# Performance work log

Measured on AMD Instinct MI355X. Metric: run time of the kernel, lower is better.

## Reference

```python
import jax, jax.numpy as jnp
import numpy as np

N_STATE = 1024
N_HEAD = 16
LENGTHS = np.array([512, 576, 640, 704, 768, 832, 896, 1024], dtype=np.int32)
BATCH = len(LENGTHS)
MAX_SEQLEN = int(LENGTHS.max())
N_CTX = int(LENGTHS.sum())


def setup_inputs() -> dict:
    key = jax.random.key(0)
    ks = jax.random.split(key, 8)
    d = N_STATE
    cu = np.concatenate([[0], np.cumsum(LENGTHS)]).astype(np.int32)
    return {
        "x": jax.random.normal(ks[0], (N_CTX, d), dtype=jnp.float32),
        "Wq": jax.random.normal(ks[1], (d, d), dtype=jnp.float32) * 0.02,
        "bq": jnp.zeros((d,), dtype=jnp.float32),
        "Wk": jax.random.normal(ks[2], (d, d), dtype=jnp.float32) * 0.02,
        "Wv": jax.random.normal(ks[3], (d, d), dtype=jnp.float32) * 0.02,
        "bv": jnp.zeros((d,), dtype=jnp.float32),
        "Wo": jax.random.normal(ks[4], (d, d), dtype=jnp.float32) * 0.02,
        "bo": jnp.zeros((d,), dtype=jnp.float32),
        "cu_seqlens": jnp.asarray(cu),
    }


def reference(x, Wq, bq, Wk, Wv, bv, Wo, bo, cu_seqlens):
    n_ctx, d = x.shape
    H, hd = N_HEAD, d // N_HEAD
    scale = hd ** -0.5
    B, S = BATCH, MAX_SEQLEN  # static pad shape

    # QKV projections (torch Linear convention: y = x @ W.T + b; key has no bias)
    q = (x @ Wq.T + bq).reshape(n_ctx, H, hd)
    k = (x @ Wk.T).reshape(n_ctx, H, hd)
    v = (x @ Wv.T + bv).reshape(n_ctx, H, hd)

    seqlens = cu_seqlens[1:] - cu_seqlens[:-1]          # [B]
    tok = jnp.arange(n_ctx)
    seg = jnp.searchsorted(cu_seqlens[1:], tok, side="right")  # [n_ctx] batch id
    pos = tok - cu_seqlens[seg]                          # [n_ctx] position in seq

    # scatter packed tokens into zero-padded [B, S, H, hd]
    qp = jnp.zeros((B, S, H, hd), q.dtype).at[seg, pos].set(q)
    kp = jnp.zeros((B, S, H, hd), k.dtype).at[seg, pos].set(k)
    vp = jnp.zeros((B, S, H, hd), v.dtype).at[seg, pos].set(v)

    valid = jnp.arange(S)[None, :] < seqlens[:, None]    # [B, S] key mask

    scores = jnp.einsum("bihd,bjhd->bhij", qp, kp) * scale   # [B, H, S, S]
    neg = -jnp.finfo(scores.dtype).max
    scores = jnp.where(valid[:, None, None, :], scores, neg)
    weights = jax.nn.softmax(scores, axis=-1)
    ctx = jnp.einsum("bhij,bjhd->bihd", weights, vp)         # [B, S, H, hd]

    # gather back to packed [n_ctx, d]
    packed = ctx[seg, pos].reshape(n_ctx, d)
    return packed @ Wo.T + bo
```

## Files before the change

### kernel.cpp

```cpp
#include <hip/hip_runtime.h>
#include <hip/hip_fp16.h>
#include <stdint.h>

#define NCTX 5952
#define NHEAD 16
#define NABLK 372
#define NWBLK 256

typedef _Float16 f16x8 __attribute__((ext_vector_type(8)));
typedef _Float16 f16x4 __attribute__((ext_vector_type(4)));
typedef float    f32x4 __attribute__((ext_vector_type(4)));

typedef const __attribute__((address_space(1))) void* gp1;
typedef __attribute__((address_space(3))) void* lp3;

__device__ __forceinline__ f32x4 mfma16(f16x8 a, f16x8 b, f32x4 c) {
    return __builtin_amdgcn_mfma_f32_16x16x32_f16(a, b, c, 0, 0, 0);
}

#define SBAR() do { __builtin_amdgcn_sched_barrier(0); \
                    __builtin_amdgcn_s_barrier();      \
                    __builtin_amdgcn_sched_barrier(0); } while (0)

__device__ const int kQT[9]    = {0, 4, 9, 14, 20, 26, 33, 40, 48};
__device__ const int kBASE8[8] = {0, 512, 1088, 1728, 2432, 3200, 4032, 4928};
__device__ const int kLEN[8]   = {512, 576, 640, 704, 768, 832, 896, 1024};


__global__ __launch_bounds__(256) void presplit_all(
    const float* __restrict__ x,
    const float* __restrict__ Wq, const float* __restrict__ Wk,
    const float* __restrict__ Wv, const float* __restrict__ Wo,
    _Float16* __restrict__ Ah, _Float16* __restrict__ Wh)
{
    constexpr int NAG = NABLK * 32 * 64;
    const int idx = blockIdx.x * 256 + threadIdx.x;
    const float* src;
    _Float16* dst;
    if (idx < NAG) {
        int chunk = idx >> 6, within = idx & 63;
        int t = chunk & 31, b = chunk >> 5;
        int rb = within >> 2, go = within & 3;
        int r = b * 16 + rb;
        int g = go ^ ((r >> 1) & 3);
        src = x + (size_t)r * 1024 + t * 32 + g * 8;
        dst = Ah + (size_t)idx * 8;
    } else {
        int i2 = idx - NAG;
        int chunk = i2 >> 6, within = i2 & 63;
        int t = chunk & 31, b = chunk >> 5;
        int rb = within >> 2, go = within & 3;
        int n = b * 16 + rb;
        int g = go ^ ((n >> 1) & 3);
        const float* s = (n < 1024) ? Wq : (n < 2048) ? Wk : (n < 3072) ? Wv : Wo;
        src = s + (size_t)(n & 1023) * 1024 + t * 32 + g * 8;
        dst = Wh + (size_t)i2 * 8;
    }
    f32x4 v0 = *(const f32x4*)src;
    f32x4 v1 = *(const f32x4*)(src + 4);
    f16x8 hv;
    #pragma unroll
    for (int e = 0; e < 4; ++e) { hv[e] = (_Float16)v0[e]; hv[4 + e] = (_Float16)v1[e]; }
    *(f16x8*)dst = hv;
}

template <int MODE>
__global__ __launch_bounds__(512) void gemm1p(
    const _Float16* __restrict__ Ag, const _Float16* __restrict__ Wg,
    const float* __restrict__ bq, const float* __restrict__ bv, const float* __restrict__ bo,
    _Float16* __restrict__ qh, _Float16* __restrict__ kh, _Float16* __restrict__ vt,
    float* __restrict__ outp)
{
    constexpr int BN   = (MODE == 0) ? 384 : 128;
    constexpr int MI   = 6;
    constexpr int NF   = BN / 64;
    constexpr int TOT  = 24 + 2 * (BN / 16);
    constexpr int SPW  = TOT / 8;
    constexpr int ABP  = 24 * 1024;
    constexpr int BUF  = ABP + (BN / 16) * 2048;
    constexpr int T    = 16;
    constexpr int WB0  = (MODE == 0) ? 0 : 192;

    __shared__ __align__(16) char lds[2 * BUF];

    int bid = blockIdx.x;
    bid = (bid & 7) * 31 + (bid >> 3);
    const int mt = bid % 31, nt = bid / 31;
    const int m0 = mt * 192, n0 = nt * BN;
    const int tid = threadIdx.x;
    const int w = tid >> 6, l = tid & 63;
    const int ls = l >> 4, lq = l & 15;
    const int wm = w >> 2, wn = w & 3;

    const char* sbase[SPW];
    int ldst[SPW];
    #pragma unroll
    for (int s = 0; s < SPW; ++s) {
        int c = w * SPW + s;
        if (c < 24) {
            int f = c >> 1, sub = c & 1;
            sbase[s] = (const char*)Ag + (size_t)(m0 / 16 + f) * 32768 + sub * 1024;
        } else {
            int cB = c - 24, f = cB >> 1, sub = cB & 1;
            sbase[s] = (const char*)Wg + (size_t)(WB0 + n0 / 16 + f) * 32768 + sub * 1024;
        }
        ldst[s] = c * 1024;
    }
    const int l16 = l * 16;
    auto STG = [&](int buf, int t2) {
        #pragma unroll
        for (int s = 0; s < SPW; ++s)
            __builtin_amdgcn_global_load_lds((gp1)(sbase[s] + (size_t)t2 * 2048 + l16),
                                             (lp3)(lds + buf * BUF + ldst[s]), 16, 0, 0);
    };

    int aoA[MI], aoB[NF];
    #pragma unroll
    for (int i = 0; i < MI; ++i) {
        int r = wm * 96 + i * 16 + lq;
        aoA[i] = (r >> 4) * 2048 + (r & 15) * 64 + ((ls ^ ((r >> 1) & 3)) << 4);
    }
    #pragma unroll
    for (int j = 0; j < NF; ++j) {
        int r = wn * (16 * NF) + j * 16 + lq;
        aoB[j] = ABP + (r >> 4) * 2048 + (r & 15) * 64 + ((ls ^ ((r >> 1) & 3)) << 4);
    }

    f32x4 acc[MI][NF] = {};

    STG(0, 0);
    asm volatile("s_waitcnt vmcnt(0)" ::: "memory");
    SBAR();

    #pragma unroll 1
    for (int t = 0; t < T; ++t) {
        const char* cbp = lds + (t & 1) * BUF;
        if (t + 1 < T) STG((t + 1) & 1, t + 1);

        #pragma unroll
        for (int kc = 0; kc < 2; ++kc) {
            f16x8 ah[MI], b[NF];
            #pragma unroll
            for (int i = 0; i < MI; ++i) ah[i] = *(const f16x8*)(cbp + aoA[i] + kc * 1024);
            #pragma unroll
            for (int j = 0; j < NF; ++j) b[j] = *(const f16x8*)(cbp + aoB[j] + kc * 1024);
            __builtin_amdgcn_s_setprio(1);
            #pragma unroll
            for (int i = 0; i < MI; ++i)
                #pragma unroll
                for (int j = 0; j < NF; ++j)
                    acc[i][j] = mfma16(ah[i], b[j], acc[i][j]);
            __builtin_amdgcn_s_setprio(0);
        }

        asm volatile("s_waitcnt vmcnt(0) lgkmcnt(0)" ::: "memory");
        SBAR();
    }

    #pragma unroll
    for (int i = 0; i < MI; ++i)
        #pragma unroll
        for (int j = 0; j < NF; ++j) {
            const int mb = m0 + wm * 96 + i * 16 + 4 * ls;
            const int n  = n0 + wn * (16 * NF) + j * 16 + lq;
            if (MODE == 0) {
                const int which = n >> 10, nn = n & 1023;
                const int hh = nn >> 6, dd = nn & 63;
                if (which == 2) {
                    f16x4 vv;
                    #pragma unroll
                    for (int r = 0; r < 4; ++r) vv[r] = (_Float16)(acc[i][j][r] + bv[nn]);
                    *(f16x4*)&vt[((size_t)hh * 64 + dd) * NCTX + mb] = vv;
                } else if (which == 0) {
                    #pragma unroll
                    for (int r = 0; r < 4; ++r)
                        qh[((size_t)hh * NCTX + mb + r) * 64 + dd] = (_Float16)(acc[i][j][r] + bq[nn]);
                } else {
                    #pragma unroll
                    for (int r = 0; r < 4; ++r)
                        kh[((size_t)hh * NCTX + mb + r) * 64 + dd] = (_Float16)acc[i][j][r];
                }
            } else {
                #pragma unroll
                for (int r = 0; r < 4; ++r)
                    outp[(size_t)(mb + r) * 1024 + n] = acc[i][j][r] + bo[n];
            }
        }
}

__global__ __launch_bounds__(256) void attn_kernel(
    const _Float16* __restrict__ qh, const _Float16* __restrict__ kh,
    const _Float16* __restrict__ vt,
    _Float16* __restrict__ Ahc)
{
    __shared__ alignas(16) _Float16 KT[2][64][64];
    __shared__ alignas(16) _Float16 VT[2][64][64];
    __shared__ alignas(16) _Float16 P[4][2][16][64];
    const int bid = blockIdx.x;
    const int hd = bid & 15, t = bid >> 4;
    int b = 0;
    while (t >= kQT[b + 1]) ++b;
    const int kbase = kBASE8[b];
    const int L = kLEN[b];
    const int w = threadIdx.x >> 6, l = threadIdx.x & 63;
    const int ls = l >> 4, lq = l & 15;
    const int xm = lq & 7;
    const int q0l = (t - kQT[b]) * 128 + w * 32;
    const bool active = (q0l < L);
    const int q0 = kbase + q0l;

    const _Float16* kb = kh + (size_t)hd * NCTX * 64;
    const _Float16* vb = vt + (size_t)hd * 64 * NCTX;

    const char* ksrc[2]; const char* vsrc[2]; int sdst[2];
    #pragma unroll
    for (int s = 0; s < 2; ++s) {
        int G = w * 128 + s * 64 + l;
        int row = G >> 3, g = G & 7;
        ksrc[s] = (const char*)(kb + ((size_t)(kbase + row)) * 64 + (size_t)((g ^ (row & 7)) * 8));
        vsrc[s] = (const char*)(vb + (size_t)row * NCTX + kbase + (size_t)((g ^ (row & 7)) * 8));
        sdst[s] = (w * 128 + s * 64) * 16;
    }
    auto STG = [&](int buf, int t2) {
        #pragma unroll
        for (int s = 0; s < 2; ++s)
            __builtin_amdgcn_global_load_lds((gp1)(ksrc[s] + (size_t)t2 * 8192),
                                             (lp3)((char*)&KT[buf][0][0] + sdst[s]), 16, 0, 0);
        #pragma unroll
        for (int s = 0; s < 2; ++s)
            __builtin_amdgcn_global_load_lds((gp1)(vsrc[s] + (size_t)t2 * 128),
                                             (lp3)((char*)&VT[buf][0][0] + sdst[s]), 16, 0, 0);
    };

    f16x8 qf[2][2];
    if (active) {
        #pragma unroll
        for (int qg = 0; qg < 2; ++qg) {
            const _Float16* qp = qh + ((size_t)hd * NCTX + q0 + qg * 16 + lq) * 64 + ls * 8;
            qf[qg][0] = *(const f16x8*)qp;
            qf[qg][1] = *(const f16x8*)(qp + 32);
        }
    }

    f32x4 acc[2][4] = {};
    float lsum[2] = {0.f, 0.f};
    const int nst = L >> 6;

    STG(0, 0);
    #pragma unroll 1
    for (int tt = 0; tt < nst; ++tt) {
        const int buf = tt & 1;
        if (tt + 1 < nst) {
            STG(buf ^ 1, tt + 1);
            asm volatile("s_waitcnt vmcnt(4)" ::: "memory");
        } else {
            asm volatile("s_waitcnt vmcnt(0)" ::: "memory");
        }
        SBAR();

        if (active) {
            f32x4 s[2][4];
            __builtin_amdgcn_s_setprio(1);
            #pragma unroll
            for (int g = 0; g < 4; ++g) {
                const char* kp = (const char*)&KT[buf][g * 16 + lq][0];
                f16x8 kf0 = *(const f16x8*)(kp + ((ls ^ xm) * 16));
                f16x8 kf1 = *(const f16x8*)(kp + (((ls + 4) ^ xm) * 16));
                #pragma unroll
                for (int qg = 0; qg < 2; ++qg) {
                    f32x4 z = {};
                    z = mfma16(kf0, qf[qg][0], z);
                    z = mfma16(kf1, qf[qg][1], z);
                    s[qg][g] = z;
                }
            }
            __builtin_amdgcn_s_setprio(0);
            #pragma unroll
            for (int qg = 0; qg < 2; ++qg) {
                float tsum = 0.f;
                #pragma unroll
                for (int g = 0; g < 4; ++g) {
                    f16x4 ph;
                    #pragma unroll
                    for (int r = 0; r < 4; ++r) {
                        float pv = __expf(s[qg][g][r] * 0.125f);
                        tsum += pv;
                        ph[r] = (_Float16)pv;
                    }
                    int gi = 2 * g + (ls >> 1);
                    *(f16x4*)&P[w][qg][lq][(((gi ^ (lq & 7)) << 3) | ((ls & 1) << 2))] = ph;
                }
                tsum += __shfl_xor(tsum, 16, 64);
                tsum += __shfl_xor(tsum, 32, 64);
                lsum[qg] += tsum;
            }
            __builtin_amdgcn_s_setprio(1);
            #pragma unroll
            for (int c = 0; c < 2; ++c) {
                f16x8 pf[2];
                #pragma unroll
                for (int qg = 0; qg < 2; ++qg)
                    pf[qg] = *(const f16x8*)&P[w][qg][lq][((4 * c + ls) ^ (lq & 7)) << 3];
                #pragma unroll
                for (int dg = 0; dg < 4; ++dg) {
                    const char* vp = (const char*)&VT[buf][dg * 16 + lq][0];
                    f16x8 vf = *(const f16x8*)(vp + (((c * 4 + ls) ^ xm) * 16));
                    #pragma unroll
                    for (int qg = 0; qg < 2; ++qg)
                        acc[qg][dg] = mfma16(vf, pf[qg], acc[qg][dg]);
                }
            }
            __builtin_amdgcn_s_setprio(0);
        }

        asm volatile("s_waitcnt lgkmcnt(0)" ::: "memory");
        SBAR();
    }

    if (active) {
        #pragma unroll
        for (int qg = 0; qg < 2; ++qg) {
            const float inv = 1.f / lsum[qg];
            const int m = q0 + qg * 16 + lq;
            const int bA = m >> 4, rbA = m & 15, xr = (m >> 1) & 3;
            #pragma unroll
            for (int dg = 0; dg < 4; ++dg) {
                const int k  = hd * 64 + dg * 16 + 4 * ls;
                const int tK = k >> 5;
                const int gs = ((k >> 3) & 3) ^ xr;
                const int e  = k & 7;
                f16x4 ch;
                #pragma unroll
                for (int r = 0; r < 4; ++r) ch[r] = (_Float16)(acc[qg][dg][r] * inv);
                *(f16x4*)((char*)Ahc + ((size_t)(bA * 32 + tK)) * 1024 + rbA * 64 + gs * 16 + e * 2) = ch;
            }
        }
    }
}

extern "C" void kernel_launch(void* const* d_in, const int* in_sizes, int n_in,
                              void* d_out, int out_size, void* d_ws, size_t ws_size,
                              hipStream_t stream)
{
    const float* x  = (const float*)d_in[0];
    const float* Wq = (const float*)d_in[1];
    const float* bq = (const float*)d_in[2];
    const float* Wk = (const float*)d_in[3];
    const float* Wv = (const float*)d_in[4];
    const float* bv = (const float*)d_in[5];
    const float* Wo = (const float*)d_in[6];
    const float* bo = (const float*)d_in[7];
    float* out = (float*)d_out;

    char* p = (char*)d_ws;
    _Float16* Ah  = (_Float16*)p; p += (size_t)NCTX * 1024 * 2;
    _Float16* Wh  = (_Float16*)p; p += (size_t)4096 * 1024 * 2;
    _Float16* qh  = (_Float16*)p; p += (size_t)NHEAD * NCTX * 64 * 2;
    _Float16* kh  = (_Float16*)p; p += (size_t)NHEAD * NCTX * 64 * 2;
    _Float16* vt  = (_Float16*)p; p += (size_t)NHEAD * NCTX * 64 * 2;
    _Float16* Ahc = (_Float16*)p; p += (size_t)NCTX * 1024 * 2;

    presplit_all<<<dim3((NABLK * 32 * 64 + NWBLK * 32 * 64) / 256), 256, 0, stream>>>(
        x, Wq, Wk, Wv, Wo, Ah, Wh);
    gemm1p<0><<<dim3(248), 512, 0, stream>>>(Ah, Wh, bq, bv, nullptr,
                                             qh, kh, vt, nullptr);
    attn_kernel<<<dim3(48 * 16), 256, 0, stream>>>(qh, kh, vt, Ahc);
    gemm1p<1><<<dim3(248), 512, 0, stream>>>(Ahc, Wh, nullptr, nullptr, bo,
                                             nullptr, nullptr, nullptr, out);
}
```

Before: 126.5 us.

## Rewrite projection GEMMs as barrier-free per-wave triple-buffered pipelines

Replaces the block-shared double-buffered GEMM with a kernel where each wave stages its own private A/B tiles into LDS, using three buffers and counted vmcnt waits instead of block barriers. Register fragments are double-buffered so LDS reads for the next k-step overlap the MFMAs of the current one. Tiles shrink to 192x192 (QKV) and 192x128 (out-proj) with 256-thread blocks, which doubles the QKV grid. Because waves no longer share tiles, global and LDS traffic goes up, and the larger per-wave LDS footprint with launch_bounds(256,1) limits occupancy.

```diff
diff --git a/kernel.cpp b/kernel.cpp
--- a/kernel.cpp
+++ b/kernel.cpp
@@ -65,106 +65,124 @@
 }
 
 template <int MODE>
-__global__ __launch_bounds__(512) void gemm1p(
+__global__ __launch_bounds__(256, 1) void gemmwp(
     const _Float16* __restrict__ Ag, const _Float16* __restrict__ Wg,
     const float* __restrict__ bq, const float* __restrict__ bv, const float* __restrict__ bo,
     _Float16* __restrict__ qh, _Float16* __restrict__ kh, _Float16* __restrict__ vt,
     float* __restrict__ outp)
 {
-    constexpr int BN   = (MODE == 0) ? 384 : 128;
-    constexpr int MI   = 6;
-    constexpr int NF   = BN / 64;
-    constexpr int TOT  = 24 + 2 * (BN / 16);
-    constexpr int SPW  = TOT / 8;
-    constexpr int ABP  = 24 * 1024;
-    constexpr int BUF  = ABP + (BN / 16) * 2048;
-    constexpr int T    = 16;
+    constexpr int BN   = (MODE == 0) ? 192 : 128;
+    constexpr int WN   = BN / 2;
+    constexpr int NJ   = WN / 16;
+    constexpr int ACH  = 6, BCH = NJ;
+    constexpr int AB   = ACH * 1024;
+    constexpr int WBUF = AB + BCH * 1024;
+    constexpr int T    = 32;
     constexpr int WB0  = (MODE == 0) ? 0 : 192;
-
-    __shared__ __align__(16) char lds[2 * BUF];
+    constexpr int NT   = (MODE == 0) ? 16 : 8;
+    constexpr int CPX  = (31 * NT) / 8;
+
+    __shared__ __align__(16) char lds[4 * 3 * WBUF];
 
     int bid = blockIdx.x;
-    bid = (bid & 7) * 31 + (bid >> 3);
+    bid = (bid & 7) * CPX + (bid >> 3);
     const int mt = bid % 31, nt = bid / 31;
-    const int m0 = mt * 192, n0 = nt * BN;
     const int tid = threadIdx.x;
     const int w = tid >> 6, l = tid & 63;
     const int ls = l >> 4, lq = l & 15;
-    const int wm = w >> 2, wn = w & 3;
-
-    const char* sbase[SPW];
-    int ldst[SPW];
-    #pragma unroll
-    for (int s = 0; s < SPW; ++s) {
-        int c = w * SPW + s;
-        if (c < 24) {
-            int f = c >> 1, sub = c & 1;
-            sbase[s] = (const char*)Ag + (size_t)(m0 / 16 + f) * 32768 + sub * 1024;
-        } else {
-            int cB = c - 24, f = cB >> 1, sub = cB & 1;
-            sbase[s] = (const char*)Wg + (size_t)(WB0 + n0 / 16 + f) * 32768 + sub * 1024;
-        }
-        ldst[s] = c * 1024;
-    }
-    const int l16 = l * 16;
+    const int wm = w >> 1, wn = w & 1;
+    const int m0 = mt * 192 + wm * 96;
+    const int n0 = nt * BN + wn * WN;
+
+    const char* asrc[ACH]; const char* bsrc[BCH];
+    #pragma unroll
+    for (int f = 0; f < ACH; ++f)
+        asrc[f] = (const char*)Ag + (size_t)(m0 / 16 + f) * 32768 + l * 16;
+    #pragma unroll
+    for (int f = 0; f < BCH; ++f)
+        bsrc[f] = (const char*)Wg + (size_t)(WB0 + n0 / 16 + f) * 32768 + l * 16;
+    char* const wlds = lds + (size_t)w * (3 * WBUF);
+
     auto STG = [&](int buf, int t2) {
-        #pragma unroll
-        for (int s = 0; s < SPW; ++s)
-            __builtin_amdgcn_global_load_lds((gp1)(sbase[s] + (size_t)t2 * 2048 + l16),
-                                             (lp3)(lds + buf * BUF + ldst[s]), 16, 0, 0);
+        char* d = wlds + buf * WBUF;
+        #pragma unroll
+        for (int f = 0; f < ACH; ++f)
+            __builtin_amdgcn_global_load_lds((gp1)(asrc[f] + (size_t)t2 * 1024),
+                                             (lp3)(d + f * 1024), 16, 0, 0);
+        #pragma unroll
+        for (int f = 0; f < BCH; ++f)
+            __builtin_amdgcn_global_load_lds((gp1)(bsrc[f] + (size_t)t2 * 1024),
+                                             (lp3)(d + AB + f * 1024), 16, 0, 0);
     };
-
-    int aoA[MI], aoB[NF];
-    #pragma unroll
-    for (int i = 0; i < MI; ++i) {
-        int r = wm * 96 + i * 16 + lq;
-        aoA[i] = (r >> 4) * 2048 + (r & 15) * 64 + ((ls ^ ((r >> 1) & 3)) << 4);
-    }
-    #pragma unroll
-    for (int j = 0; j < NF; ++j) {
-        int r = wn * (16 * NF) + j * 16 + lq;
-        aoB[j] = ABP + (r >> 4) * 2048 + (r & 15) * 64 + ((ls ^ ((r >> 1) & 3)) << 4);
-    }
-
-    f32x4 acc[MI][NF] = {};
+    #define VMN() do { if constexpr (MODE == 0) asm volatile("s_waitcnt vmcnt(12)" ::: "memory"); \
+                       else                     asm volatile("s_waitcnt vmcnt(10)" ::: "memory"); } while (0)
+    #define VM0() asm volatile("s_waitcnt vmcnt(0)" ::: "memory")
+
+    const int swz = (ls ^ ((lq >> 1) & 3)) << 4;
+    int aoA[6], aoB[NJ];
+    #pragma unroll
+    for (int i = 0; i < 6; ++i) aoA[i] = i * 1024 + lq * 64 + swz;
+    #pragma unroll
+    for (int j = 0; j < NJ; ++j) aoB[j] = AB + j * 1024 + lq * 64 + swz;
+
+    f32x4 acc[6][NJ] = {};
+    f16x8 a0[6], b0[NJ], a1[6], b1[NJ];
 
     STG(0, 0);
-    asm volatile("s_waitcnt vmcnt(0)" ::: "memory");
-    SBAR();
-
+    STG(1, 1);
+    VMN();
+    #pragma unroll
+    for (int i = 0; i < 6; ++i) a0[i] = *(const f16x8*)(wlds + aoA[i]);
+    #pragma unroll
+    for (int j = 0; j < NJ; ++j) b0[j] = *(const f16x8*)(wlds + aoB[j]);
+
+    int c = 0, n = 1, p = 2;
     #pragma unroll 1
-    for (int t = 0; t < T; ++t) {
-        const char* cbp = lds + (t & 1) * BUF;
-        if (t + 1 < T) STG((t + 1) & 1, t + 1);
-
-        #pragma unroll
-        for (int kc = 0; kc < 2; ++kc) {
-            f16x8 ah[MI], b[NF];
-            #pragma unroll
-            for (int i = 0; i < MI; ++i) ah[i] = *(const f16x8*)(cbp + aoA[i] + kc * 1024);
-            #pragma unroll
-            for (int j = 0; j < NF; ++j) b[j] = *(const f16x8*)(cbp + aoB[j] + kc * 1024);
-            __builtin_amdgcn_s_setprio(1);
-            #pragma unroll
-            for (int i = 0; i < MI; ++i)
-                #pragma unroll
-                for (int j = 0; j < NF; ++j)
-                    acc[i][j] = mfma16(ah[i], b[j], acc[i][j]);
-            __builtin_amdgcn_s_setprio(0);
-        }
-
-        asm volatile("s_waitcnt vmcnt(0) lgkmcnt(0)" ::: "memory");
-        SBAR();
-    }
-
-    #pragma unroll
-    for (int i = 0; i < MI; ++i)
-        #pragma unroll
-        for (int j = 0; j < NF; ++j) {
-            const int mb = m0 + wm * 96 + i * 16 + 4 * ls;
-            const int n  = n0 + wn * (16 * NF) + j * 16 + lq;
+    for (int t = 0; t < T; t += 2) {
+        if (t + 2 < T) { STG(p, t + 2); VMN(); }
+        else           { VM0(); }
+        {
+            const char* pn = wlds + n * WBUF;
+            #pragma unroll
+            for (int i = 0; i < 6; ++i) a1[i] = *(const f16x8*)(pn + aoA[i]);
+            #pragma unroll
+            for (int j = 0; j < NJ; ++j) b1[j] = *(const f16x8*)(pn + aoB[j]);
+        }
+        #pragma unroll
+        for (int i = 0; i < 6; ++i)
+            #pragma unroll
+            for (int j = 0; j < NJ; ++j)
+                acc[i][j] = mfma16(a0[i], b0[j], acc[i][j]);
+
+        if (t + 3 < T)      { STG(c, t + 3); VMN(); }
+        else if (t + 2 < T) { VM0(); }
+        if (t + 2 < T) {
+            const char* pp = wlds + p * WBUF;
+            #pragma unroll
+            for (int i = 0; i < 6; ++i) a0[i] = *(const f16x8*)(pp + aoA[i]);
+            #pragma unroll
+            for (int j = 0; j < NJ; ++j) b0[j] = *(const f16x8*)(pp + aoB[j]);
+        }
+        #pragma unroll
+        for (int i = 0; i < 6; ++i)
+            #pragma unroll
+            for (int j = 0; j < NJ; ++j)
+                acc[i][j] = mfma16(a1[i], b1[j], acc[i][j]);
+
+        int oc = c, on = n, op = p;
+        c = op; n = oc; p = on;
+    }
+    #undef VMN
+    #undef VM0
+
+    #pragma unroll
+    for (int i = 0; i < 6; ++i)
+        #pragma unroll
+        for (int j = 0; j < NJ; ++j) {
+            const int mb = m0 + i * 16 + 4 * ls;
+            const int nn2 = n0 + j * 16 + lq;
             if (MODE == 0) {
-                const int which = n >> 10, nn = n & 1023;
+                const int which = nn2 >> 10, nn = nn2 & 1023;
                 const int hh = nn >> 6, dd = nn & 63;
                 if (which == 2) {
                     f16x4 vv;
@@ -183,7 +201,7 @@
             } else {
                 #pragma unroll
                 for (int r = 0; r < 4; ++r)
-                    outp[(size_t)(mb + r) * 1024 + n] = acc[i][j][r] + bo[n];
+                    outp[(size_t)(mb + r) * 1024 + nn2] = acc[i][j][r] + bo[nn2];
             }
         }
 }
@@ -362,9 +380,9 @@
 
     presplit_all<<<dim3((NABLK * 32 * 64 + NWBLK * 32 * 64) / 256), 256, 0, stream>>>(
         x, Wq, Wk, Wv, Wo, Ah, Wh);
-    gemm1p<0><<<dim3(248), 512, 0, stream>>>(Ah, Wh, bq, bv, nullptr,
-                                             qh, kh, vt, nullptr);
+    gemmwp<0><<<dim3(31 * 16), 256, 0, stream>>>(Ah, Wh, bq, bv, nullptr,
+                                                 qh, kh, vt, nullptr);
     attn_kernel<<<dim3(48 * 16), 256, 0, stream>>>(qh, kh, vt, Ahc);
-    gemm1p<1><<<dim3(248), 512, 0, stream>>>(Ahc, Wh, nullptr, nullptr, bo,
-                                             nullptr, nullptr, nullptr, out);
-}
+    gemmwp<1><<<dim3(31 * 8), 256, 0, stream>>>(Ahc, Wh, nullptr, nullptr, bo,
+                                                nullptr, nullptr, nullptr, out);
+}
```

Measured after the change: 139.1 us. +9.9%, slower.
